# Kernel tuning notes

Measured on AMD Instinct MI355X. Metric: run time of the kernel, lower is better.

Reference implementation:

```python
import jax, jax.numpy as jnp
import numpy as np

EPS = 1e-6

def setup_inputs() -> dict:
    key = jax.random.key(0)
    ks = jax.random.split(key, 8)
    I, S, O = 1024, 512, 1024
    Bsz, T = 4, 2048
    return {
        "u": jax.random.normal(ks[0], (Bsz, T, I), dtype=jnp.float32),
        "dt": jax.random.normal(ks[1], (S,), dtype=jnp.float32),
        "A": jax.random.normal(ks[2], (S,), dtype=jnp.float32),
        "Bmat": jax.random.normal(ks[3], (I, S), dtype=jnp.float32) / np.sqrt(S),
        "C": jax.random.normal(ks[4], (S, O), dtype=jnp.float32) / np.sqrt(S),
        "D": jax.random.normal(ks[5], (O,), dtype=jnp.float32),
        "norm_w": jnp.ones((I,), dtype=jnp.float32),
    }

def _rmsnorm(x, w):
    x32 = x.astype(jnp.float32)
    n = x32 * jax.lax.rsqrt(jnp.mean(x32 * x32, axis=-1, keepdims=True) + EPS)
    return n.astype(x.dtype) * w

def reference(u, dt, A, Bmat, C, D, norm_w):
    u = _rmsnorm(u, norm_w)                      # [B, T, I]
    Bsz, T, _ = u.shape
    dts = jax.nn.sigmoid(dt)                     # [S]
    a = jnp.exp(-dts * jnp.abs(A))               # [S] discretized decay
    t = jnp.arange(T, dtype=jnp.float32)
    h = dts[:, None] * a[:, None] ** t[None, :]  # [S, T] geometric kernel
    u_proj = jnp.einsum('bti,is->bst', u, Bmat)  # [B, S, T]
    # depthwise causal conv: flipped kernel + cross-correlation == convolution
    k = jnp.flip(h, axis=1)[:, None, :]          # [S, 1, T] (OIW)
    x = jax.lax.conv_general_dilated(
        u_proj, k, window_strides=(1,), padding=[(T - 1, T - 1)],
        dimension_numbers=('NCW', 'OIW', 'NCW'),
        feature_group_count=u_proj.shape[1])[:, :, :T]  # [B, S, T]
    x = jnp.transpose(x, (0, 2, 1))              # [B, T, S]
    y = jnp.einsum('bts,so->bto', x, C) + D      # [B, T, O]
    return (y, x[:, -1])
```

## Files before the change

kernel.cpp:

```cpp
#include <hip/hip_runtime.h>
#include <math.h>

#define I_DIM 1024
#define S_DIM 512
#define O_DIM 1024
#define T_DIM 2048
#define B_SZ 4
#define M_ROWS (B_SZ * T_DIM)
#define EPSF 1e-6f

#define CL 64
#define NCH 32

typedef _Float16 f16;
typedef __attribute__((ext_vector_type(8))) _Float16 f16x8;
typedef __attribute__((ext_vector_type(2))) _Float16 f16x2;
typedef __attribute__((ext_vector_type(4))) float f32x4;

__device__ __forceinline__ unsigned short f2h_bits(float f) {
    _Float16 h = (_Float16)f;
    return __builtin_bit_cast(unsigned short, h);
}

__device__ __forceinline__ void load16_lds(const void* g, void* l) {
    __builtin_amdgcn_global_load_lds((const __attribute__((address_space(1))) void*)g,
                                     (__attribute__((address_space(3))) void*)l,
                                     16, 0, 0);
}

__global__ __launch_bounds__(256)
void prep_w(const float* __restrict__ Bmat, const float* __restrict__ dt,
            const float* __restrict__ nw, unsigned short* __restrict__ Bt16,
            const float* __restrict__ Cmat, unsigned short* __restrict__ Ct16) {
    __shared__ float tile[32][33];
    const int t = threadIdx.x;
    const int tx = t & 31, ty = t >> 5;
    const int bx = blockIdx.x;
    if (bx < 512) {
        const int bs = (bx & 15) * 32;
        const int bi = (bx >> 4) * 32;
        #pragma unroll
        for (int i = ty; i < 32; i += 8)
            tile[i][tx] = Bmat[(size_t)(bi + i) * S_DIM + bs + tx];
        __syncthreads();
        const float w = nw[bi + tx];
        #pragma unroll
        for (int i = ty; i < 32; i += 8) {
            const int s = bs + i;
            const float dts = 1.0f / (1.0f + expf(-dt[s]));
            Bt16[(size_t)s * I_DIM + bi + tx] = f2h_bits(tile[tx][i] * dts * w);
        }
    } else {
        const int tb = bx - 512;
        const int bo = (tb & 31) * 32;
        const int bs = (tb >> 5) * 32;
        #pragma unroll
        for (int i = ty; i < 32; i += 8)
            tile[i][tx] = Cmat[(size_t)(bs + i) * O_DIM + bo + tx];
        __syncthreads();
        #pragma unroll
        for (int i = ty; i < 32; i += 8)
            Ct16[(size_t)(bo + i) * S_DIM + bs + tx] = f2h_bits(tile[tx][i]);
    }
}

__global__ __launch_bounds__(256)
void gemm1_rms_chfin(const float* __restrict__ U, const f16* __restrict__ Bt,
                     f16* __restrict__ up, float* __restrict__ chlast,
                     const float* __restrict__ dt, const float* __restrict__ Avec) {
    constexpr int K = I_DIM, N = S_DIM, NK = K / 32;
    __shared__ f16 As[3][64 * 32];
    __shared__ f16 Bs[3][128 * 32];
    __shared__ float rsbuf[64];
    const int t = threadIdx.x;

    int bid = blockIdx.x;
    bid = (bid & 7) * 64 + (bid >> 3);
    const int n0 = (bid & 3) * 128;
    const int m0 = (bid >> 2) * 64;
    const int wid = t >> 6, lane = t & 63;
    const int wn = wid * 32, lr = lane & 15, kg = lane >> 4;

    const int swch = (t & 3) ^ ((t >> 3) & 3);
    const float* aptr = U + (size_t)(m0 + (t >> 2)) * K + swch * 8;
    const f16*  bptr = Bt + (size_t)(n0 + (t >> 2)) * K + swch * 8;
    const int rchunk = (kg ^ ((lr >> 1) & 3)) * 8;
    f16* adst = (f16*)&As[0][0] + t * 8;

    float ss = 0.f;
    f32x4 acc[4][2];
    #pragma unroll
    for (int i = 0; i < 4; ++i)
        #pragma unroll
        for (int j = 0; j < 2; ++j) acc[i][j] = (f32x4){0.f, 0.f, 0.f, 0.f};

    float4 Ar0[2], Ar1[2], Ar2[2];
    auto aset = [&](int i) -> float4* { return i == 0 ? Ar0 : (i == 1 ? Ar1 : Ar2); };

    auto loadA = [&](int kt, float4* r) {
        r[0] = *(const float4*)(aptr + kt * 32);
        r[1] = *(const float4*)(aptr + kt * 32 + 4);
    };
    auto stageB = [&](int kt, int slot) {
        load16_lds(bptr + kt * 32, &Bs[slot][t * 8]);
        load16_lds(bptr + (size_t)64 * K + kt * 32, &Bs[slot][2048 + t * 8]);
    };
    auto writeA = [&](const float4* r, int slot) {
        ss += r[0].x * r[0].x + r[0].y * r[0].y + r[0].z * r[0].z + r[0].w * r[0].w
            + r[1].x * r[1].x + r[1].y * r[1].y + r[1].z * r[1].z + r[1].w * r[1].w;
        f16x8 h = { (_Float16)r[0].x, (_Float16)r[0].y, (_Float16)r[0].z, (_Float16)r[0].w,
                    (_Float16)r[1].x, (_Float16)r[1].y, (_Float16)r[1].z, (_Float16)r[1].w };
        *(f16x8*)(adst + slot * 2048) = h;
    };

    loadA(0, Ar0); stageB(0, 0);
    loadA(1, Ar1); stageB(1, 1);
    loadA(2, Ar2);
    asm volatile("s_waitcnt vmcnt(8)");
    writeA(Ar0, 0);

    #pragma unroll
    for (int kt = 0; kt < NK; ++kt) {
        asm volatile("s_waitcnt lgkmcnt(0)");
        if (kt <= NK - 3)      asm volatile("s_waitcnt vmcnt(4)");
        else if (kt == NK - 2) asm volatile("s_waitcnt vmcnt(2)");
        else                   asm volatile("s_waitcnt vmcnt(0)");
        __builtin_amdgcn_s_barrier();
        __builtin_amdgcn_sched_barrier(0);

        if (kt + 1 < NK) writeA(aset((kt + 1) % 3), (kt + 1) % 3);
        if (kt + 3 < NK) loadA(kt + 3, aset((kt + 3) % 3));
        if (kt + 2 < NK) stageB(kt + 2, (kt + 2) % 3);

        const int slot = kt % 3;
        f16x8 af[4], bf[2];
        #pragma unroll
        for (int m = 0; m < 4; ++m)
            af[m] = *(const f16x8*)&As[slot][(m * 16 + lr) * 32 + rchunk];
        #pragma unroll
        for (int n = 0; n < 2; ++n)
            bf[n] = *(const f16x8*)&Bs[slot][(wn + n * 16 + lr) * 32 + rchunk];
        __builtin_amdgcn_s_setprio(1);
        #pragma unroll
        for (int m = 0; m < 4; ++m)
            #pragma unroll
            for (int n = 0; n < 2; ++n)
                acc[m][n] = __builtin_amdgcn_mfma_f32_16x16x32_f16(af[m], bf[n], acc[m][n], 0, 0, 0);
        __builtin_amdgcn_s_setprio(0);
    }

    ss += __shfl_xor(ss, 1, 64);
    ss += __shfl_xor(ss, 2, 64);
    if ((t & 3) == 0) rsbuf[t >> 2] = rsqrtf(ss * (1.0f / K) + EPSF);
    __syncthreads();

    const int cb = m0 >> 11;
    const int cc = (m0 >> 6) & (NCH - 1);
    #pragma unroll
    for (int n = 0; n < 2; ++n) {
        const int col = n0 + wn + n * 16 + lr;
        const float dts = 1.0f / (1.0f + expf(-dt[col]));
        const float e = dts * fabsf(Avec[col]);
        const float ainv = expf(e);
        float partial = 0.f;
        #pragma unroll
        for (int m = 0; m < 4; ++m) {
            const int row = m * 16 + kg * 4;
            f32x4 rs4 = *(const f32x4*)&rsbuf[row];
            float wgt = expf(-e * (float)(63 - row));
            #pragma unroll
            for (int j = 0; j < 4; ++j) {
                const float val = rs4[j] * acc[m][n][j];
                up[(size_t)(m0 + row + j) * N + col] = (_Float16)val;
                partial = fmaf(wgt, val, partial);
                wgt *= ainv;
            }
        }
        partial += __shfl_xor(partial, 16, 64);
        partial += __shfl_xor(partial, 32, 64);
        if (kg == 0)
            chlast[(size_t)(cb * NCH + cc) * S_DIM + col] = partial;
    }
}

__global__ __launch_bounds__(256)
void gemm2_scan(const f16* __restrict__ upb, const float* __restrict__ chlast,
                const f16* __restrict__ Ct, const float* __restrict__ Dvec,
                const float* __restrict__ dt, const float* __restrict__ Avec,
                float* __restrict__ y, float* __restrict__ xlast) {
    constexpr int K = S_DIM, N = O_DIM, NK = K / 32;
    __shared__ __align__(16) unsigned char As[64 * 1024];
    __shared__ f16 Bs[2][128 * 32];
    const int t = threadIdx.x;

    int bid = blockIdx.x;
    bid = (bid & 7) * 128 + (bid >> 3);
    const int n0 = (bid & 7) * 128;
    const int m0 = (bid >> 3) * 64;
    const int wid = t >> 6, lane = t & 63;
    const int wn = wid * 32, lr = lane & 15, kg = lane >> 4;

    const int srcswz = ((t & 3) ^ ((t >> 3) & 3)) * 8;
    const f16* bptr = Ct + (size_t)(n0 + (t >> 2)) * K + srcswz;
    auto stageB = [&](int kt, int slot) {
        load16_lds(bptr + kt * 32, &Bs[slot][t * 8]);
        load16_lds(bptr + (size_t)64 * K + kt * 32, &Bs[slot][2048 + t * 8]);
    };
    stageB(0, 0);
    const int rchunk = (kg ^ ((lr >> 1) & 3)) * 8;

    const int cc = (m0 >> 6) & (NCH - 1);
    const int cb = m0 >> 11;
    const int s0 = 2 * t;
    const float dts0 = 1.0f / (1.0f + expf(-dt[s0]));
    const float dts1 = 1.0f / (1.0f + expf(-dt[s0 + 1]));
    const float ab0 = fabsf(Avec[s0]), ab1 = fabsf(Avec[s0 + 1]);
    const float g0 = expf(-dts0 * ab0);
    const float g1 = expf(-dts1 * ab1);
    const float gCL0 = expf(-dts0 * ab0 * (float)CL);
    const float gCL1 = expf(-dts1 * ab1 * (float)CL);
    const float2* ch = (const float2*)chlast;
    float cy0 = 0.f, cy1 = 0.f;
    {
        int j = 0;
        for (; j + 4 <= cc; j += 4) {
            float2 f0 = ch[(size_t)(cb * NCH + j + 0) * 256 + t];
            float2 f1 = ch[(size_t)(cb * NCH + j + 1) * 256 + t];
            float2 f2 = ch[(size_t)(cb * NCH + j + 2) * 256 + t];
            float2 f3 = ch[(size_t)(cb * NCH + j + 3) * 256 + t];
            cy0 = fmaf(gCL0, cy0, f0.x); cy1 = fmaf(gCL1, cy1, f0.y);
            cy0 = fmaf(gCL0, cy0, f1.x); cy1 = fmaf(gCL1, cy1, f1.y);
            cy0 = fmaf(gCL0, cy0, f2.x); cy1 = fmaf(gCL1, cy1, f2.y);
            cy0 = fmaf(gCL0, cy0, f3.x); cy1 = fmaf(gCL1, cy1, f3.y);
        }
        for (; j < cc; ++j) {
            float2 f = ch[(size_t)(cb * NCH + j) * 256 + t];
            cy0 = fmaf(gCL0, cy0, f.x);
            cy1 = fmaf(gCL1, cy1, f.y);
        }
    }

    const unsigned* up32 = (const unsigned*)upb;
    const size_t ub = (size_t)m0 * 256 + t;
    unsigned v[CL];
    #pragma unroll
    for (int j = 0; j < CL; ++j) v[j] = up32[ub + (size_t)j * 256];
    float x0 = cy0, x1 = cy1;
    #pragma unroll
    for (int j = 0; j < CL; ++j) {
        f16x2 h = __builtin_bit_cast(f16x2, v[j]);
        x0 = fmaf(g0, x0, (float)h.x);
        x1 = fmaf(g1, x1, (float)h.y);
        f16x2 o; o.x = (_Float16)x0; o.y = (_Float16)x1;
        v[j] = __builtin_bit_cast(unsigned, o);
    }
    #pragma unroll
    for (int j = 0; j < CL; ++j)
        *(unsigned*)&As[j * 1024 + ((t * 4) ^ ((j & 7) << 4))] = v[j];
    if (cc == NCH - 1)
        ((float2*)xlast)[cb * 256 + t] = make_float2(x0, x1);
    __syncthreads();

    f32x4 acc[4][2];
    #pragma unroll
    for (int i = 0; i < 4; ++i)
        #pragma unroll
        for (int j = 0; j < 2; ++j) acc[i][j] = (f32x4){0.f, 0.f, 0.f, 0.f};

    const int swz = (lr & 7) << 4;
    for (int kt = 0; kt < NK; ++kt) {
        const int cur = kt & 1;
        if (kt + 1 < NK) {
            stageB(kt + 1, cur ^ 1);
            asm volatile("s_waitcnt vmcnt(2)");
        } else {
            asm volatile("s_waitcnt vmcnt(0)");
        }
        __builtin_amdgcn_s_barrier();
        __builtin_amdgcn_sched_barrier(0);

        f16x8 af[4], bf[2];
        #pragma unroll
        for (int m = 0; m < 4; ++m)
            af[m] = *(const f16x8*)&As[(m * 16 + lr) * 1024 + ((kt * 64 + kg * 16) ^ swz)];
        #pragma unroll
        for (int n = 0; n < 2; ++n)
            bf[n] = *(const f16x8*)&Bs[cur][(wn + n * 16 + lr) * 32 + rchunk];
        #pragma unroll
        for (int m = 0; m < 4; ++m)
            #pragma unroll
            for (int n = 0; n < 2; ++n)
                acc[m][n] = __builtin_amdgcn_mfma_f32_16x16x32_f16(af[m], bf[n], acc[m][n], 0, 0, 0);
        __builtin_amdgcn_s_barrier();
    }

    #pragma unroll
    for (int n = 0; n < 2; ++n) {
        const int col = n0 + wn + n * 16 + lr;
        const float dv = Dvec[col];
        #pragma unroll
        for (int m = 0; m < 4; ++m) {
            const int row = m0 + m * 16 + kg * 4;
            #pragma unroll
            for (int j = 0; j < 4; ++j)
                y[(size_t)(row + j) * N + col] = acc[m][n][j] + dv;
        }
    }
}

extern "C" void kernel_launch(void* const* d_in, const int* in_sizes, int n_in,
                              void* d_out, int out_size, void* d_ws, size_t ws_size,
                              hipStream_t stream) {
    const float* u    = (const float*)d_in[0];
    const float* dt   = (const float*)d_in[1];
    const float* Avec = (const float*)d_in[2];
    const float* Bmat = (const float*)d_in[3];
    const float* Cmat = (const float*)d_in[4];
    const float* Dvec = (const float*)d_in[5];
    const float* nw   = (const float*)d_in[6];

    float* y     = (float*)d_out;
    float* xlast = y + (size_t)M_ROWS * O_DIM;

    char* w = (char*)d_ws;
    f16*            up16   = (f16*)(w);
    unsigned short* Bt16   = (unsigned short*)(w + 8388608);
    unsigned short* Ct16   = (unsigned short*)(w + 9437184);
    float*          chlast = (float*)(w + 10485760);

    prep_w<<<1024, 256, 0, stream>>>(Bmat, dt, nw, Bt16, Cmat, Ct16);

    gemm1_rms_chfin<<<512, 256, 0, stream>>>(u, (const f16*)Bt16, up16, chlast, dt, Avec);

    gemm2_scan<<<1024, 256, 0, stream>>>(up16, chlast, (const f16*)Ct16, Dvec,
                                         dt, Avec, y, xlast);
}
```

Measured before the change: 55.49 us.

## Widen GEMM1 K-tile to 64 with new LDS swizzle; hoist scan loads earlier

GEMM1 now uses a K-step of 64 instead of 32, which halves the number of barrier iterations. It adds a new XOR swizzle for the A and B LDS tiles and splits each tile into two MFMA sub-steps. In the second kernel, the 64 chunk loads of up are issued before the carry-in recurrence over chunk-last values, so their latency overlaps that loop, and s_setprio is added around its MFMAs. LDS use for the triple-buffered tiles doubles and more registers are held live, which may cut occupancy.

```diff
diff --git a/kernel.cpp b/kernel.cpp
--- a/kernel.cpp
+++ b/kernel.cpp
@@ -68,9 +68,9 @@
 void gemm1_rms_chfin(const float* __restrict__ U, const f16* __restrict__ Bt,
                      f16* __restrict__ up, float* __restrict__ chlast,
                      const float* __restrict__ dt, const float* __restrict__ Avec) {
-    constexpr int K = I_DIM, N = S_DIM, NK = K / 32;
-    __shared__ f16 As[3][64 * 32];
-    __shared__ f16 Bs[3][128 * 32];
+    constexpr int K = I_DIM, N = S_DIM, NK = K / 64;
+    __shared__ f16 As[3][64 * 64];
+    __shared__ f16 Bs[3][128 * 64];
     __shared__ float rsbuf[64];
     const int t = threadIdx.x;
 
@@ -81,11 +81,16 @@
     const int wid = t >> 6, lane = t & 63;
     const int wn = wid * 32, lr = lane & 15, kg = lane >> 4;
 
-    const int swch = (t & 3) ^ ((t >> 3) & 3);
-    const float* aptr = U + (size_t)(m0 + (t >> 2)) * K + swch * 8;
-    const f16*  bptr = Bt + (size_t)(n0 + (t >> 2)) * K + swch * 8;
-    const int rchunk = (kg ^ ((lr >> 1) & 3)) * 8;
-    f16* adst = (f16*)&As[0][0] + t * 8;
+    const int arow = t >> 2;
+    const int fra = arow & 7;
+    const int swzA0 = (2 * (t & 3)) ^ fra;
+    const int swzA1 = (2 * (t & 3) + 1) ^ fra;
+    const float* aptr = U + (size_t)(m0 + arow) * K;
+    f16* adst = (f16*)&As[0][0] + arow * 64 + (t & 3) * 16;
+
+    const int bsw = (t & 7) ^ ((t >> 3) & 7);
+    const f16* bptr = Bt + (size_t)(n0 + (t >> 3)) * K + bsw * 8;
+    const int rchunk = lr & 7;
 
     float ss = 0.f;
     f32x4 acc[4][2];
@@ -94,36 +99,44 @@
         #pragma unroll
         for (int j = 0; j < 2; ++j) acc[i][j] = (f32x4){0.f, 0.f, 0.f, 0.f};
 
-    float4 Ar0[2], Ar1[2], Ar2[2];
+    float4 Ar0[4], Ar1[4], Ar2[4];
     auto aset = [&](int i) -> float4* { return i == 0 ? Ar0 : (i == 1 ? Ar1 : Ar2); };
 
     auto loadA = [&](int kt, float4* r) {
-        r[0] = *(const float4*)(aptr + kt * 32);
-        r[1] = *(const float4*)(aptr + kt * 32 + 4);
+        const float* p = aptr + kt * 64;
+        r[0] = *(const float4*)(p + swzA0 * 8);
+        r[1] = *(const float4*)(p + swzA0 * 8 + 4);
+        r[2] = *(const float4*)(p + swzA1 * 8);
+        r[3] = *(const float4*)(p + swzA1 * 8 + 4);
     };
     auto stageB = [&](int kt, int slot) {
-        load16_lds(bptr + kt * 32, &Bs[slot][t * 8]);
-        load16_lds(bptr + (size_t)64 * K + kt * 32, &Bs[slot][2048 + t * 8]);
+        #pragma unroll
+        for (int q = 0; q < 4; ++q)
+            load16_lds(bptr + (size_t)(q * 32) * K + kt * 64, &Bs[slot][q * 2048 + t * 8]);
     };
     auto writeA = [&](const float4* r, int slot) {
-        ss += r[0].x * r[0].x + r[0].y * r[0].y + r[0].z * r[0].z + r[0].w * r[0].w
-            + r[1].x * r[1].x + r[1].y * r[1].y + r[1].z * r[1].z + r[1].w * r[1].w;
-        f16x8 h = { (_Float16)r[0].x, (_Float16)r[0].y, (_Float16)r[0].z, (_Float16)r[0].w,
-                    (_Float16)r[1].x, (_Float16)r[1].y, (_Float16)r[1].z, (_Float16)r[1].w };
-        *(f16x8*)(adst + slot * 2048) = h;
+        #pragma unroll
+        for (int i = 0; i < 4; ++i)
+            ss += r[i].x * r[i].x + r[i].y * r[i].y + r[i].z * r[i].z + r[i].w * r[i].w;
+        f16x8 h0 = { (_Float16)r[0].x, (_Float16)r[0].y, (_Float16)r[0].z, (_Float16)r[0].w,
+                     (_Float16)r[1].x, (_Float16)r[1].y, (_Float16)r[1].z, (_Float16)r[1].w };
+        f16x8 h1 = { (_Float16)r[2].x, (_Float16)r[2].y, (_Float16)r[2].z, (_Float16)r[2].w,
+                     (_Float16)r[3].x, (_Float16)r[3].y, (_Float16)r[3].z, (_Float16)r[3].w };
+        *(f16x8*)(adst + slot * 4096) = h0;
+        *(f16x8*)(adst + slot * 4096 + 8) = h1;
     };
 
     loadA(0, Ar0); stageB(0, 0);
     loadA(1, Ar1); stageB(1, 1);
     loadA(2, Ar2);
-    asm volatile("s_waitcnt vmcnt(8)");
+    asm volatile("s_waitcnt vmcnt(16)");
     writeA(Ar0, 0);
 
     #pragma unroll
     for (int kt = 0; kt < NK; ++kt) {
         asm volatile("s_waitcnt lgkmcnt(0)");
-        if (kt <= NK - 3)      asm volatile("s_waitcnt vmcnt(4)");
-        else if (kt == NK - 2) asm volatile("s_waitcnt vmcnt(2)");
+        if (kt <= NK - 3)      asm volatile("s_waitcnt vmcnt(8)");
+        else if (kt == NK - 2) asm volatile("s_waitcnt vmcnt(4)");
         else                   asm volatile("s_waitcnt vmcnt(0)");
         __builtin_amdgcn_s_barrier();
         __builtin_amdgcn_sched_barrier(0);
@@ -133,20 +146,24 @@
         if (kt + 2 < NK) stageB(kt + 2, (kt + 2) % 3);
 
         const int slot = kt % 3;
-        f16x8 af[4], bf[2];
-        #pragma unroll
-        for (int m = 0; m < 4; ++m)
-            af[m] = *(const f16x8*)&As[slot][(m * 16 + lr) * 32 + rchunk];
-        #pragma unroll
-        for (int n = 0; n < 2; ++n)
-            bf[n] = *(const f16x8*)&Bs[slot][(wn + n * 16 + lr) * 32 + rchunk];
-        __builtin_amdgcn_s_setprio(1);
-        #pragma unroll
-        for (int m = 0; m < 4; ++m)
+        #pragma unroll
+        for (int sub = 0; sub < 2; ++sub) {
+            const int rc = ((sub * 4 + kg) ^ rchunk) * 8;
+            f16x8 af[4], bf[2];
+            #pragma unroll
+            for (int m = 0; m < 4; ++m)
+                af[m] = *(const f16x8*)&As[slot][(m * 16 + lr) * 64 + rc];
             #pragma unroll
             for (int n = 0; n < 2; ++n)
-                acc[m][n] = __builtin_amdgcn_mfma_f32_16x16x32_f16(af[m], bf[n], acc[m][n], 0, 0, 0);
-        __builtin_amdgcn_s_setprio(0);
+                bf[n] = *(const f16x8*)&Bs[slot][(wn + n * 16 + lr) * 64 + rc];
+            __builtin_amdgcn_s_setprio(1);
+            #pragma unroll
+            for (int m = 0; m < 4; ++m)
+                #pragma unroll
+                for (int n = 0; n < 2; ++n)
+                    acc[m][n] = __builtin_amdgcn_mfma_f32_16x16x32_f16(af[m], bf[n], acc[m][n], 0, 0, 0);
+            __builtin_amdgcn_s_setprio(0);
+        }
     }
 
     ss += __shfl_xor(ss, 1, 64);
@@ -208,6 +225,12 @@
     };
     stageB(0, 0);
     const int rchunk = (kg ^ ((lr >> 1) & 3)) * 8;
+
+    const unsigned* up32 = (const unsigned*)upb;
+    const size_t ub = (size_t)m0 * 256 + t;
+    unsigned v[CL];
+    #pragma unroll
+    for (int j = 0; j < CL; ++j) v[j] = up32[ub + (size_t)j * 256];
 
     const int cc = (m0 >> 6) & (NCH - 1);
     const int cb = m0 >> 11;
@@ -240,11 +263,6 @@
         }
     }
 
-    const unsigned* up32 = (const unsigned*)upb;
-    const size_t ub = (size_t)m0 * 256 + t;
-    unsigned v[CL];
-    #pragma unroll
-    for (int j = 0; j < CL; ++j) v[j] = up32[ub + (size_t)j * 256];
     float x0 = cy0, x1 = cy1;
     #pragma unroll
     for (int j = 0; j < CL; ++j) {
@@ -286,11 +304,13 @@
         #pragma unroll
         for (int n = 0; n < 2; ++n)
             bf[n] = *(const f16x8*)&Bs[cur][(wn + n * 16 + lr) * 32 + rchunk];
+        __builtin_amdgcn_s_setprio(1);
         #pragma unroll
         for (int m = 0; m < 4; ++m)
             #pragma unroll
             for (int n = 0; n < 2; ++n)
                 acc[m][n] = __builtin_amdgcn_mfma_f32_16x16x32_f16(af[m], bf[n], acc[m][n], 0, 0, 0);
+        __builtin_amdgcn_s_setprio(0);
         __builtin_amdgcn_s_barrier();
     }
 
```

Result: faster. 54.35 us (-2.1%).

## Stage A in 256-wide K slabs in gemm1 and hoist up loads in gemm2

Applied to the files above, without the earlier changes.

gemm1 drops the triple-buffered per-32-K A pipeline. Each thread now issues 16 float4 loads covering a 256-wide K slab, converts them to f16 into a large swizzled LDS buffer, and runs 8 MFMA k-steps over it with double-buffered B staging. The aim is fewer barriers per A element and more loads in flight. The cost is more registers and LDS, and A load latency is exposed between slabs instead of being pipelined. gemm2 moves the chunk-input global loads ahead of the carry computation so they overlap it, and adds setprio around its MFMAs.

```diff
diff --git a/kernel.cpp b/kernel.cpp
--- a/kernel.cpp
+++ b/kernel.cpp
@@ -68,9 +68,9 @@
 void gemm1_rms_chfin(const float* __restrict__ U, const f16* __restrict__ Bt,
                      f16* __restrict__ up, float* __restrict__ chlast,
                      const float* __restrict__ dt, const float* __restrict__ Avec) {
-    constexpr int K = I_DIM, N = S_DIM, NK = K / 32;
-    __shared__ f16 As[3][64 * 32];
-    __shared__ f16 Bs[3][128 * 32];
+    constexpr int K = I_DIM, N = S_DIM;
+    __shared__ f16 As[64 * 256];
+    __shared__ f16 Bs[2][128 * 32];
     __shared__ float rsbuf[64];
     const int t = threadIdx.x;
 
@@ -81,72 +81,78 @@
     const int wid = t >> 6, lane = t & 63;
     const int wn = wid * 32, lr = lane & 15, kg = lane >> 4;
 
+    const int ar_row = t >> 2;
+    const float* aptr = U + (size_t)(m0 + ar_row) * K + (t & 3) * 64;
+    const int r7 = ar_row & 7;
+    const int gchk0 = (t & 3) * 8;
+
     const int swch = (t & 3) ^ ((t >> 3) & 3);
-    const float* aptr = U + (size_t)(m0 + (t >> 2)) * K + swch * 8;
-    const f16*  bptr = Bt + (size_t)(n0 + (t >> 2)) * K + swch * 8;
-    const int rchunk = (kg ^ ((lr >> 1) & 3)) * 8;
-    f16* adst = (f16*)&As[0][0] + t * 8;
-
-    float ss = 0.f;
-    f32x4 acc[4][2];
-    #pragma unroll
-    for (int i = 0; i < 4; ++i)
-        #pragma unroll
-        for (int j = 0; j < 2; ++j) acc[i][j] = (f32x4){0.f, 0.f, 0.f, 0.f};
-
-    float4 Ar0[2], Ar1[2], Ar2[2];
-    auto aset = [&](int i) -> float4* { return i == 0 ? Ar0 : (i == 1 ? Ar1 : Ar2); };
-
-    auto loadA = [&](int kt, float4* r) {
-        r[0] = *(const float4*)(aptr + kt * 32);
-        r[1] = *(const float4*)(aptr + kt * 32 + 4);
-    };
+    const f16* bptr = Bt + (size_t)(n0 + (t >> 2)) * K + swch * 8;
+    const int rchunkB = (kg ^ ((lr >> 1) & 3)) * 8;
+    const int axor = lr & 7;
+
     auto stageB = [&](int kt, int slot) {
         load16_lds(bptr + kt * 32, &Bs[slot][t * 8]);
         load16_lds(bptr + (size_t)64 * K + kt * 32, &Bs[slot][2048 + t * 8]);
     };
-    auto writeA = [&](const float4* r, int slot) {
-        ss += r[0].x * r[0].x + r[0].y * r[0].y + r[0].z * r[0].z + r[0].w * r[0].w
-            + r[1].x * r[1].x + r[1].y * r[1].y + r[1].z * r[1].z + r[1].w * r[1].w;
-        f16x8 h = { (_Float16)r[0].x, (_Float16)r[0].y, (_Float16)r[0].z, (_Float16)r[0].w,
-                    (_Float16)r[1].x, (_Float16)r[1].y, (_Float16)r[1].z, (_Float16)r[1].w };
-        *(f16x8*)(adst + slot * 2048) = h;
-    };
-
-    loadA(0, Ar0); stageB(0, 0);
-    loadA(1, Ar1); stageB(1, 1);
-    loadA(2, Ar2);
-    asm volatile("s_waitcnt vmcnt(8)");
-    writeA(Ar0, 0);
-
-    #pragma unroll
-    for (int kt = 0; kt < NK; ++kt) {
+
+    float ss = 0.f;
+    f32x4 acc[4][2];
+    #pragma unroll
+    for (int i = 0; i < 4; ++i)
+        #pragma unroll
+        for (int j = 0; j < 2; ++j) acc[i][j] = (f32x4){0.f, 0.f, 0.f, 0.f};
+
+    #pragma unroll
+    for (int q = 0; q < 4; ++q) {
+        float4 ar[16];
+        #pragma unroll
+        for (int j = 0; j < 16; ++j)
+            ar[j] = *(const float4*)(aptr + q * 256 + j * 4);
+        stageB(q * 8, 0);
+        asm volatile("s_waitcnt vmcnt(2)");
+
+        #pragma unroll
+        for (int c = 0; c < 8; ++c) {
+            const float4 a0 = ar[2 * c], a1 = ar[2 * c + 1];
+            ss += a0.x * a0.x + a0.y * a0.y + a0.z * a0.z + a0.w * a0.w
+                + a1.x * a1.x + a1.y * a1.y + a1.z * a1.z + a1.w * a1.w;
+            f16x8 h = { (_Float16)a0.x, (_Float16)a0.y, (_Float16)a0.z, (_Float16)a0.w,
+                        (_Float16)a1.x, (_Float16)a1.y, (_Float16)a1.z, (_Float16)a1.w };
+            const int ldc = (gchk0 + c) ^ r7;
+            *(f16x8*)&As[ar_row * 256 + ldc * 8] = h;
+        }
         asm volatile("s_waitcnt lgkmcnt(0)");
-        if (kt <= NK - 3)      asm volatile("s_waitcnt vmcnt(4)");
-        else if (kt == NK - 2) asm volatile("s_waitcnt vmcnt(2)");
-        else                   asm volatile("s_waitcnt vmcnt(0)");
         __builtin_amdgcn_s_barrier();
-        __builtin_amdgcn_sched_barrier(0);
-
-        if (kt + 1 < NK) writeA(aset((kt + 1) % 3), (kt + 1) % 3);
-        if (kt + 3 < NK) loadA(kt + 3, aset((kt + 3) % 3));
-        if (kt + 2 < NK) stageB(kt + 2, (kt + 2) % 3);
-
-        const int slot = kt % 3;
-        f16x8 af[4], bf[2];
-        #pragma unroll
-        for (int m = 0; m < 4; ++m)
-            af[m] = *(const f16x8*)&As[slot][(m * 16 + lr) * 32 + rchunk];
-        #pragma unroll
-        for (int n = 0; n < 2; ++n)
-            bf[n] = *(const f16x8*)&Bs[slot][(wn + n * 16 + lr) * 32 + rchunk];
-        __builtin_amdgcn_s_setprio(1);
-        #pragma unroll
-        for (int m = 0; m < 4; ++m)
+
+        #pragma unroll
+        for (int ks = 0; ks < 8; ++ks) {
+            const int cur = ks & 1;
+            if (ks < 7) {
+                stageB(q * 8 + ks + 1, cur ^ 1);
+                asm volatile("s_waitcnt vmcnt(2)");
+            } else {
+                asm volatile("s_waitcnt vmcnt(0)");
+            }
+            __builtin_amdgcn_s_barrier();
+            __builtin_amdgcn_sched_barrier(0);
+
+            f16x8 af[4], bf[2];
+            #pragma unroll
+            for (int m = 0; m < 4; ++m)
+                af[m] = *(const f16x8*)&As[(m * 16 + lr) * 256 + (((ks * 4 + kg) ^ axor) * 8)];
             #pragma unroll
             for (int n = 0; n < 2; ++n)
-                acc[m][n] = __builtin_amdgcn_mfma_f32_16x16x32_f16(af[m], bf[n], acc[m][n], 0, 0, 0);
-        __builtin_amdgcn_s_setprio(0);
+                bf[n] = *(const f16x8*)&Bs[cur][(wn + n * 16 + lr) * 32 + rchunkB];
+            __builtin_amdgcn_s_setprio(1);
+            #pragma unroll
+            for (int m = 0; m < 4; ++m)
+                #pragma unroll
+                for (int n = 0; n < 2; ++n)
+                    acc[m][n] = __builtin_amdgcn_mfma_f32_16x16x32_f16(af[m], bf[n], acc[m][n], 0, 0, 0);
+            __builtin_amdgcn_s_setprio(0);
+            __builtin_amdgcn_s_barrier();
+        }
     }
 
     ss += __shfl_xor(ss, 1, 64);
@@ -208,6 +214,12 @@
     };
     stageB(0, 0);
     const int rchunk = (kg ^ ((lr >> 1) & 3)) * 8;
+
+    const unsigned* up32 = (const unsigned*)upb;
+    const size_t ub = (size_t)m0 * 256 + t;
+    unsigned v[CL];
+    #pragma unroll
+    for (int j = 0; j < CL; ++j) v[j] = up32[ub + (size_t)j * 256];
 
     const int cc = (m0 >> 6) & (NCH - 1);
     const int cb = m0 >> 11;
@@ -240,11 +252,6 @@
         }
     }
 
-    const unsigned* up32 = (const unsigned*)upb;
-    const size_t ub = (size_t)m0 * 256 + t;
-    unsigned v[CL];
-    #pragma unroll
-    for (int j = 0; j < CL; ++j) v[j] = up32[ub + (size_t)j * 256];
     float x0 = cy0, x1 = cy1;
     #pragma unroll
     for (int j = 0; j < CL; ++j) {
@@ -286,11 +293,13 @@
         #pragma unroll
         for (int n = 0; n < 2; ++n)
             bf[n] = *(const f16x8*)&Bs[cur][(wn + n * 16 + lr) * 32 + rchunk];
+        __builtin_amdgcn_s_setprio(1);
         #pragma unroll
         for (int m = 0; m < 4; ++m)
             #pragma unroll
             for (int n = 0; n < 2; ++n)
                 acc[m][n] = __builtin_amdgcn_mfma_f32_16x16x32_f16(af[m], bf[n], acc[m][n], 0, 0, 0);
+        __builtin_amdgcn_s_setprio(0);
         __builtin_amdgcn_s_barrier();
     }
 
```

Result: slower. 67.67 us (+21.9%).
